# Optimization experiments

Hardware: AMD Instinct MI355X
Metric: run time of the kernel (lower is better)

## Reference

```python
import jax, jax.numpy as jnp
import numpy as np

H = 16  # n_head
EPS = 1e-12  # F.normalize eps


def l2norm(t):
    n = jnp.linalg.norm(t, axis=-1, keepdims=True)
    return t / jnp.maximum(n, EPS)


def setup_inputs() -> dict:
    key = jax.random.key(0)
    ks = jax.random.split(key, 12)
    B, T, C, K, N = 4, 1024, 1024, 16, 16384
    T_xl = 1024
    return {
        "x": jax.random.normal(ks[0], (B, T, C), jnp.float32),
        "xl_memory": jax.random.normal(ks[1], (B, T_xl, 2, C), jnp.float32),
        "relative_positions": jax.random.normal(ks[2], (H, T, T_xl + T), jnp.float32),
        "db": jax.random.normal(ks[3], (B, N, 2, C), jnp.float32),
        "knn_idx": jax.random.randint(ks[4], (B, T, K), 0, N, jnp.int32),
        "knn_mask": jnp.ones((B,), bool),
        "Wq": jax.random.normal(ks[5], (C, C), jnp.float32) * (C ** -0.5),
        "Wk": jax.random.normal(ks[6], (C, C), jnp.float32) * (C ** -0.5),
        "Wv": jax.random.normal(ks[7], (C, C), jnp.float32) * (C ** -0.5),
        "Wp": jax.random.normal(ks[8], (C, C), jnp.float32) * (C ** -0.5),
        "bp": jnp.zeros((C,), jnp.float32),
        "gate_bias": jax.random.normal(ks[9], (H, 1, 1), jnp.float32),
    }


def reference(x, xl_memory, relative_positions, db, knn_idx, knn_mask,
              Wq, Wk, Wv, Wp, bp, gate_bias):
    B, T, C = x.shape
    D = C // H
    scale = D ** -0.5

    # projections (torch Linear: y = x @ W.T), then L2-normalize q, k
    q = l2norm(jnp.einsum('btc,oc->bto', x, Wq))
    k = l2norm(jnp.einsum('btc,oc->bto', x, Wk))
    v = jnp.einsum('btc,oc->bto', x, Wv)

    k_xl, v_xl = xl_memory[..., 0, :], xl_memory[..., 1, :]
    k_full = jnp.concatenate((k_xl, k), axis=1)   # [B, j, C]
    v_full = jnp.concatenate((v_xl, v), axis=1)

    def to_heads(t):  # [B, S, C] -> [B, H, S, D]
        return t.reshape(B, t.shape[1], H, D).transpose(0, 2, 1, 3)

    qh, kh, vh = to_heads(q), to_heads(k_full), to_heads(v_full)
    i, j = T, k_full.shape[1]

    # XL attention with relative bias, scale applied AFTER bias (as in source)
    w = jnp.einsum('bhid,bhjd->bhij', qh, kh)
    w = (w + relative_positions[None, :, -i:, -j:]) * scale
    causal = jnp.triu(jnp.ones((i, j), bool), j - i + 1)
    w = jnp.where(causal, -jnp.inf, w)
    w = jax.nn.softmax(w, axis=-1)
    weighted_values = jnp.einsum('bhij,bhjd->bhid', w, vh)  # [B,H,T,D]

    # kNN memory attention: per-token gather of top-k (key,value) pairs
    mem_kv = db[jnp.arange(B)[:, None, None], knn_idx]      # [B,T,K,2,C]
    Kk = knn_idx.shape[-1]
    mem_k = mem_kv[..., 0, :].reshape(B, T, Kk, H, D).transpose(0, 3, 1, 2, 4)  # [B,H,T,K,D]
    mem_v = mem_kv[..., 1, :].reshape(B, T, Kk, H, D).transpose(0, 3, 1, 2, 4)
    mem_w = jnp.einsum('bhtd,bhtkd->bhtk', qh, mem_k) * scale
    mem_w = jax.nn.softmax(mem_w, axis=-1)
    mem_weighted = jnp.einsum('bhtk,bhtkd->bhtd', mem_w, mem_v)

    # per-head gated combination, then per-batch knn availability mask
    g = gate_bias[None]  # [1,H,1,1]
    combined = mem_weighted * g + weighted_values * (1.0 - g)
    combined = jnp.where(knn_mask[:, None, None, None], combined, weighted_values)

    out = combined.transpose(0, 2, 1, 3).reshape(B, T, C)
    out = jnp.einsum('btc,oc->bto', out, Wp) + bp

    # new XL memory: last T (normalized-k, v) pairs
    new_xl_memory = jnp.stack((k_full, v_full), axis=-2)[:, -T:]  # [B,T,2,C]
    return out, new_xl_memory
```

## Files before the change

kernel.cpp:

```cpp
#include <hip/hip_runtime.h>

typedef unsigned short u16;
typedef float f32x4 __attribute__((ext_vector_type(4)));
typedef u16 u16x4 __attribute__((ext_vector_type(4)));
typedef u16 u16x8 __attribute__((ext_vector_type(8)));
typedef __bf16 bf16x8 __attribute__((ext_vector_type(8)));

#define QSCALE 0.18033688011112043f

__device__ __forceinline__ u16 f2b(float f) {
    unsigned u = __float_as_uint(f);
    unsigned r = (u + 0x7fffu + ((u >> 16) & 1u)) >> 16;
    return (u16)r;
}

__device__ __forceinline__ float b2f(u16 v) {
    return __uint_as_float((unsigned)v << 16);
}

__device__ __forceinline__ int tile_ofs(int qb) {
    return 17 * qb + (qb * (qb - 1)) / 2;
}

__device__ __forceinline__ f32x4 mfma16(u16x8 a, u16x8 b, f32x4 c) {
    return __builtin_amdgcn_mfma_f32_16x16x32_bf16(
        __builtin_bit_cast(bf16x8, a), __builtin_bit_cast(bf16x8, b), c, 0, 0, 0);
}

__device__ __forceinline__ void gload_lds16(const void* g, void* l) {
    __builtin_amdgcn_global_load_lds(
        (const __attribute__((address_space(1))) void*)g,
        (__attribute__((address_space(3))) void*)l, 16, 0, 0);
}

__global__ __launch_bounds__(256) void convert_all_kernel(
    const float* __restrict__ x, const float* __restrict__ Wq,
    const float* __restrict__ Wk, const float* __restrict__ Wv,
    const float* __restrict__ Wp, const float* __restrict__ xl,
    const float* __restrict__ rel,
    u16* __restrict__ x_b, u16* __restrict__ Wcat, u16* __restrict__ Wpb,
    u16* __restrict__ kf, u16* __restrict__ vf, u16* __restrict__ relt) {
    int i = blockIdx.x * 256 + threadIdx.x;
    if (i < 4194304) {
        const float* src;
        u16* dst;
        if (i < 1048576) {
            src = x + 4 * (size_t)i;
            dst = x_b + 4 * (size_t)i;
        } else if (i < 1835008) {
            int j = i - 1048576;
            int sel = j >> 18, off = j & 262143;
            const float* s = sel == 0 ? Wq : sel == 1 ? Wk : Wv;
            src = s + 4 * (size_t)off;
            dst = Wcat + 4 * (size_t)j;
        } else if (i < 2097152) {
            int j = i - 1835008;
            src = Wp + 4 * (size_t)j;
            dst = Wpb + 4 * (size_t)j;
        } else {
            int j = i - 2097152;
            int c4 = j & 255, s = (j >> 8) & 1, t = (j >> 9) & 1023, b = j >> 19;
            src = xl + 4 * (size_t)j;
            dst = (s == 0 ? kf : vf) + ((size_t)b * 2048 + t) * 1024 + c4 * 4;
        }
        f32x4 v = *(const f32x4*)src;
        u16x4 o;
        o[0] = f2b(v[0]); o[1] = f2b(v[1]); o[2] = f2b(v[2]); o[3] = f2b(v[3]);
        *(u16x4*)dst = o;
    } else {
        int g = i - 4194304;
        int ftid = g & 255;
        int lin = g >> 8;
        int h = lin / 392;
        int lt = lin - h * 392;
        int qb = 0;
#pragma unroll
        for (int q = 1; q < 16; ++q)
            if (lt >= tile_ofs(q)) qb = q;
        int jt = lt - tile_ofs(qb);
        int w = ftid >> 6, lane = ftid & 63, g16 = lane >> 4, l16 = lane & 15;
        const float* rbase = rel + ((size_t)h * 1024 + qb * 64 + w * 16 + g16 * 4) * 2048
                                 + jt * 64 + l16;
        u16 vals[16];
#pragma unroll
        for (int nj = 0; nj < 4; ++nj)
#pragma unroll
            for (int r2 = 0; r2 < 4; ++r2)
                vals[nj * 4 + r2] = f2b(rbase[(size_t)r2 * 2048 + nj * 16] * QSCALE);
        u16* dstp = relt + ((size_t)lin * 256 + ftid) * 16;
        *(u16x8*)dstp = *(u16x8*)vals;
        *(u16x8*)(dstp + 8) = *(u16x8*)(vals + 8);
    }
}

__global__ __launch_bounds__(256) void gemm_bt_kernel(const u16* __restrict__ A,
                                                      const u16* __restrict__ B,
                                                      float* __restrict__ C,
                                                      u16* __restrict__ Cb,
                                                      int M, int N, int K,
                                                      const float* __restrict__ bias) {
    __shared__ u16 As[2][128 * 32];
    __shared__ u16 Bs[2][128 * 32];
    const int tid = threadIdx.x;
    const int w = tid >> 6, lane = tid & 63, g16 = lane >> 4, l16 = lane & 15;
    const int wr = w >> 1, wc = w & 1;
    const int m0 = blockIdx.y * 128, n0 = blockIdx.x * 128;

    f32x4 acc[4][4];
    f32x4 z4 = {0.f, 0.f, 0.f, 0.f};
#pragma unroll
    for (int mi = 0; mi < 4; ++mi)
#pragma unroll
        for (int nj = 0; nj < 4; ++nj) acc[mi][nj] = z4;

    const int r0 = tid >> 2;
    const int koff = (tid & 3) * 8;

    for (int k0 = 0; k0 < K; k0 += 64) {
#pragma unroll
        for (int half = 0; half < 2; ++half)
#pragma unroll
            for (int s = 0; s < 2; ++s) {
                int rr = r0 + 64 * s;
                gload_lds16(A + (size_t)(m0 + rr) * K + k0 + half * 32 + koff,
                            (char*)As[half] + w * 1024 + s * 4096);
                gload_lds16(B + (size_t)(n0 + rr) * K + k0 + half * 32 + koff,
                            (char*)Bs[half] + w * 1024 + s * 4096);
            }
        __syncthreads();
#pragma unroll
        for (int half = 0; half < 2; ++half) {
            u16x8 af[4], bfr[4];
#pragma unroll
            for (int x = 0; x < 4; ++x) {
                af[x]  = *(const u16x8*)&As[half][(wr * 64 + x * 16 + l16) * 32 + g16 * 8];
                bfr[x] = *(const u16x8*)&Bs[half][(wc * 64 + x * 16 + l16) * 32 + g16 * 8];
            }
#pragma unroll
            for (int mi = 0; mi < 4; ++mi)
#pragma unroll
                for (int nj = 0; nj < 4; ++nj)
                    acc[mi][nj] = mfma16(af[mi], bfr[nj], acc[mi][nj]);
        }
        __syncthreads();
    }

#pragma unroll
    for (int mi = 0; mi < 4; ++mi) {
        int row = m0 + wr * 64 + mi * 16 + g16 * 4;
#pragma unroll
        for (int nj = 0; nj < 4; ++nj) {
            int col = n0 + wc * 64 + nj * 16 + l16;
            if (Cb) {
#pragma unroll
                for (int rr = 0; rr < 4; ++rr)
                    Cb[(size_t)(row + rr) * N + col] = f2b(acc[mi][nj][rr]);
            } else {
                float bval = bias ? bias[col] : 0.0f;
#pragma unroll
                for (int rr = 0; rr < 4; ++rr)
                    C[(size_t)(row + rr) * N + col] = acc[mi][nj][rr] + bval;
            }
        }
    }
}

__global__ __launch_bounds__(256) void postproc_kernel(const u16* __restrict__ qkvb,
                                                       u16* __restrict__ qb16,
                                                       u16* __restrict__ kfull,
                                                       u16* __restrict__ vfull,
                                                       float* __restrict__ newxl) {
    int row = blockIdx.x;
    int b = row >> 10, t = row & 1023;
    int tid = threadIdx.x, w = tid >> 6, lane = tid & 63;
    const u16* qr = qkvb + (size_t)row * 3072;

    u16x4 q4 = ((const u16x4*)qr)[tid];
    u16x4 k4 = ((const u16x4*)(qr + 1024))[tid];
    u16x4 v4 = ((const u16x4*)(qr + 2048))[tid];
    float qa[4], ka[4], va[4];
    float sq = 0.f, sk = 0.f;
#pragma unroll
    for (int j = 0; j < 4; ++j) {
        qa[j] = b2f(q4[j]); sq += qa[j] * qa[j];
        ka[j] = b2f(k4[j]); sk += ka[j] * ka[j];
        va[j] = b2f(v4[j]);
    }
#pragma unroll
    for (int mk = 32; mk; mk >>= 1) {
        sq += __shfl_xor(sq, mk);
        sk += __shfl_xor(sk, mk);
    }
    __shared__ float red[2][4];
    if (lane == 0) { red[0][w] = sq; red[1][w] = sk; }
    __syncthreads();
    sq = red[0][0] + red[0][1] + red[0][2] + red[0][3];
    sk = red[1][0] + red[1][1] + red[1][2] + red[1][3];
    float rq = QSCALE / fmaxf(sqrtf(sq), 1e-12f);
    float rk = 1.0f / fmaxf(sqrtf(sk), 1e-12f);

    size_t orow = (size_t)row * 1024;
    size_t krow = ((size_t)b * 2048 + 1024 + t) * 1024;
    size_t xrow = (size_t)row * 2048;
    u16x4 qo, ko;
    f32x4 kx, vx;
#pragma unroll
    for (int j = 0; j < 4; ++j) {
        qo[j] = f2b(qa[j] * rq);
        float kv = ka[j] * rk;
        ko[j] = f2b(kv);
        kx[j] = kv;
        vx[j] = va[j];
    }
    ((u16x4*)(qb16 + orow))[tid] = qo;
    ((u16x4*)(kfull + krow))[tid] = ko;
    ((u16x4*)(vfull + krow))[tid] = v4;
    ((f32x4*)(newxl + xrow))[tid] = kx;
    ((f32x4*)(newxl + xrow + 1024))[tid] = vx;
}

__global__ __launch_bounds__(256) void flash_kernel(const u16* __restrict__ qb16,
                                                    const u16* __restrict__ kfull,
                                                    const u16* __restrict__ vfull,
                                                    const u16* __restrict__ relt,
                                                    u16* __restrict__ wvout) {
    const int qb = blockIdx.x, h = blockIdx.y, b = blockIdx.z;
    const int tid = threadIdx.x, w = tid >> 6, lane = tid & 63;
    const int g16 = lane >> 4, l16 = lane & 15;
    __shared__ u16 Ks[2][64 * 64];
    __shared__ u16 Vt[2][64 * 64];
    __shared__ u16 Ps[4][16 * 64];
    const int qi0 = qb * 64;

    {
        const u16* base = qb16 + ((size_t)(b * 1024 + qi0)) * 1024 + h * 64;
#pragma unroll
        for (int s = 0; s < 2; ++s) {
            int off = (tid + 256 * s) * 16;
            int r = off >> 7, cb = off & 127;
            int cbs = cb ^ ((r & 7) << 4);
            gload_lds16((const char*)(base + (size_t)r * 1024) + cbs,
                        (char*)Ks[0] + w * 1024 + s * 4096);
        }
    }
    __syncthreads();
    u16x8 qf[2];
#pragma unroll
    for (int ks = 0; ks < 2; ++ks) {
        int row = w * 16 + l16;
        int cb = (ks * 64 + g16 * 16) ^ ((row & 7) << 4);
        qf[ks] = *(const u16x8*)((const char*)Ks[0] + row * 128 + cb);
    }
    __syncthreads();

    auto stageK = [&](int buf, int j0) {
        const u16* kbase = kfull + ((size_t)b * 2048 + j0) * 1024 + h * 64;
#pragma unroll
        for (int s = 0; s < 2; ++s) {
            int off = (tid + 256 * s) * 16;
            int r = off >> 7, cb = off & 127;
            int cbs = cb ^ ((r & 7) << 4);
            gload_lds16((const char*)(kbase + (size_t)r * 1024) + cbs,
                        (char*)Ks[buf] + w * 1024 + s * 4096);
        }
    };
    const int jp = tid >> 3, d0v = (tid & 7) * 8;
    auto loadV = [&](int j0, u16x8* v0, u16x8* v1) {
        const u16* v0p = vfull + ((size_t)b * 2048 + j0 + 2 * jp) * 1024 + h * 64 + d0v;
        *v0 = *(const u16x8*)v0p;
        *v1 = *(const u16x8*)(v0p + 1024);
    };
    auto writeVt = [&](int buf, u16x8 v0, u16x8 v1) {
#pragma unroll
        for (int u = 0; u < 8; ++u) {
            int d = d0v + u;
            unsigned val = (unsigned)v0[u] | ((unsigned)v1[u] << 16);
            int bo = d * 128 + ((4 * jp) ^ ((d & 7) << 4));
            *(unsigned*)((char*)Vt[buf] + bo) = val;
        }
    };

    const u16* relp = relt + ((size_t)(h * 392 + tile_ofs(qb)) * 256 + tid) * 16;

    float l_r[4] = {0.f, 0.f, 0.f, 0.f};
    f32x4 accO[4];
    f32x4 z4 = {0.f, 0.f, 0.f, 0.f};
#pragma unroll
    for (int nd = 0; nd < 4; ++nd) accO[nd] = z4;

    const int ntiles = qb + 17;
    u16x8 v0n, v1n, rc0, rc1, rn0, rn1;

    stageK(0, 0);
    loadV(0, &v0n, &v1n);
    rc0 = *(const u16x8*)relp;
    rc1 = *(const u16x8*)(relp + 8);
    __syncthreads();
    writeVt(0, v0n, v1n);
    __syncthreads();

    int cur = 0;
    for (int jt = 0; jt < ntiles; ++jt) {
        const int j0 = jt * 64;
        const bool more = (jt + 1 < ntiles);
        if (more) {
            stageK(cur ^ 1, j0 + 64);
            loadV(j0 + 64, &v0n, &v1n);
            const u16* rp = relp + (size_t)(jt + 1) * 256 * 16;
            rn0 = *(const u16x8*)rp;
            rn1 = *(const u16x8*)(rp + 8);
        }

        f32x4 s4[4];
#pragma unroll
        for (int nj = 0; nj < 4; ++nj) {
            u16x8 rc = (nj < 2) ? rc0 : rc1;
            int base4 = (nj & 1) * 4;
            s4[nj][0] = b2f(rc[base4 + 0]);
            s4[nj][1] = b2f(rc[base4 + 1]);
            s4[nj][2] = b2f(rc[base4 + 2]);
            s4[nj][3] = b2f(rc[base4 + 3]);
#pragma unroll
            for (int ks = 0; ks < 2; ++ks) {
                int row = nj * 16 + l16;
                int cb = (ks * 64 + g16 * 16) ^ ((row & 7) << 4);
                u16x8 kf = *(const u16x8*)((const char*)Ks[cur] + row * 128 + cb);
                s4[nj] = mfma16(qf[ks], kf, s4[nj]);
            }
        }

        if (more) {
#pragma unroll
            for (int nj = 0; nj < 4; ++nj)
#pragma unroll
                for (int r2 = 0; r2 < 4; ++r2) {
                    float pe = exp2f(s4[nj][r2]);
                    l_r[r2] += pe;
                    int prow = g16 * 4 + r2;
                    int pbo = prow * 128 + (((nj * 16 + l16) * 2) ^ ((prow & 7) << 4));
                    *(u16*)((char*)Ps[w] + pbo) = __builtin_bit_cast(u16, (__bf16)pe);
                }
        } else {
#pragma unroll
            for (int nj = 0; nj < 4; ++nj) {
                int jg = j0 + nj * 16 + l16;
#pragma unroll
                for (int r2 = 0; r2 < 4; ++r2) {
                    int ig = qi0 + w * 16 + g16 * 4 + r2;
                    float pe = (jg > ig + 1024) ? 0.f : exp2f(s4[nj][r2]);
                    l_r[r2] += pe;
                    int prow = g16 * 4 + r2;
                    int pbo = prow * 128 + (((nj * 16 + l16) * 2) ^ ((prow & 7) << 4));
                    *(u16*)((char*)Ps[w] + pbo) = __builtin_bit_cast(u16, (__bf16)pe);
                }
            }
        }

#pragma unroll
        for (int ks = 0; ks < 2; ++ks) {
            int acb = (ks * 64 + g16 * 16) ^ ((l16 & 7) << 4);
            u16x8 pf = *(const u16x8*)((const char*)Ps[w] + l16 * 128 + acb);
#pragma unroll
            for (int nd = 0; nd < 4; ++nd) {
                int brow = nd * 16 + l16;
                int bcb = (ks * 64 + g16 * 16) ^ ((brow & 7) << 4);
                u16x8 vf = *(const u16x8*)((const char*)Vt[cur] + brow * 128 + bcb);
                accO[nd] = mfma16(pf, vf, accO[nd]);
            }
        }

        if (more) {
            writeVt(cur ^ 1, v0n, v1n);
            rc0 = rn0; rc1 = rn1;
        }
        __syncthreads();
        cur ^= 1;
    }

#pragma unroll
    for (int r2 = 0; r2 < 4; ++r2) {
#pragma unroll
        for (int mk = 1; mk < 16; mk <<= 1) l_r[r2] += __shfl_xor(l_r[r2], mk);
        l_r[r2] = __builtin_amdgcn_rcpf(l_r[r2]);
    }

#pragma unroll
    for (int nd = 0; nd < 4; ++nd)
#pragma unroll
        for (int r2 = 0; r2 < 4; ++r2) {
            int ig = qi0 + w * 16 + g16 * 4 + r2;
            int col = h * 64 + nd * 16 + l16;
            wvout[((size_t)b * 1024 + ig) * 1024 + col] = f2b(accO[nd][r2] * l_r[r2]);
        }
}

__global__ __launch_bounds__(256) void memgate_kernel(const u16* __restrict__ qb16,
                                                      const float* __restrict__ db,
                                                      const int* __restrict__ knn,
                                                      const u16* __restrict__ wvbuf,
                                                      const float* __restrict__ gate,
                                                      u16* __restrict__ comb) {
    int blk = blockIdx.x;
    int b = blk >> 10;
    int tid = threadIdx.x, w = tid >> 6, lane = tid & 63;
    int h = w * 4 + (lane >> 4);
    int l16 = lane & 15;
    int d0base = h * 64 + l16 * 4;
    size_t rowoff = (size_t)blk * 1024 + d0base;

    u16x4 qv = *(const u16x4*)(qb16 + rowoff);
    f32x4 q4;
    q4[0] = b2f(qv[0]); q4[1] = b2f(qv[1]); q4[2] = b2f(qv[2]); q4[3] = b2f(qv[3]);
    const int* kidx = knn + (size_t)blk * 16;

    float logit[16];
#pragma unroll
    for (int kk = 0; kk < 16; ++kk) {
        size_t roff = ((size_t)b * 16384 + kidx[kk]) * 2048 + d0base;
        f32x4 k4 = *(const f32x4*)(db + roff);
        float pp = q4[0] * k4[0] + q4[1] * k4[1] + q4[2] * k4[2] + q4[3] * k4[3];
        pp += __shfl_xor(pp, 1);
        pp += __shfl_xor(pp, 2);
        pp += __shfl_xor(pp, 4);
        pp += __shfl_xor(pp, 8);
        logit[kk] = pp;
    }
    float mx = -1e30f;
#pragma unroll
    for (int kk = 0; kk < 16; ++kk) mx = fmaxf(mx, logit[kk]);
    float ssum = 0.f;
    float pr[16];
#pragma unroll
    for (int kk = 0; kk < 16; ++kk) {
        pr[kk] = exp2f(logit[kk] - mx);
        ssum += pr[kk];
    }
    float inv = __builtin_amdgcn_rcpf(ssum);
    f32x4 acc = {0.f, 0.f, 0.f, 0.f};
#pragma unroll
    for (int kk = 0; kk < 16; ++kk) {
        size_t roff = ((size_t)b * 16384 + kidx[kk]) * 2048 + 1024 + d0base;
        f32x4 v4 = *(const f32x4*)(db + roff);
        float pw = pr[kk] * inv;
        acc[0] += pw * v4[0];
        acc[1] += pw * v4[1];
        acc[2] += pw * v4[2];
        acc[3] += pw * v4[3];
    }
    u16x4 wv4 = *(const u16x4*)(wvbuf + rowoff);
    float g = gate[h];
    u16x4 o;
#pragma unroll
    for (int j = 0; j < 4; ++j) o[j] = f2b(acc[j] * g + b2f(wv4[j]) * (1.f - g));
    *(u16x4*)(comb + rowoff) = o;
}

extern "C" void kernel_launch(void* const* d_in, const int* in_sizes, int n_in,
                              void* d_out, int out_size, void* d_ws, size_t ws_size,
                              hipStream_t stream) {
    const float* x    = (const float*)d_in[0];
    const float* xl   = (const float*)d_in[1];
    const float* rel  = (const float*)d_in[2];
    const float* db   = (const float*)d_in[3];
    const int*   knn  = (const int*)d_in[4];
    const float* Wq   = (const float*)d_in[6];
    const float* Wk   = (const float*)d_in[7];
    const float* Wv   = (const float*)d_in[8];
    const float* Wp   = (const float*)d_in[9];
    const float* bp   = (const float*)d_in[10];
    const float* gate = (const float*)d_in[11];

    float* out   = (float*)d_out;
    float* newxl = out + (size_t)4 * 1024 * 1024;

    char* p = (char*)d_ws;
    auto alloc = [&](size_t bytes) {
        char* q = p;
        p += (bytes + 255) & ~(size_t)255;
        return q;
    };
    u16*   x_b    = (u16*)alloc((size_t)4096 * 1024 * 2);
    u16*   Wcat_b = (u16*)alloc((size_t)3072 * 1024 * 2);
    u16*   Wp_b   = (u16*)alloc((size_t)1024 * 1024 * 2);
    u16*   rel_t  = (u16*)alloc((size_t)16 * 392 * 256 * 16 * 2);
    u16*   qkvb   = (u16*)alloc((size_t)4096 * 3072 * 2);
    u16*   q_b    = (u16*)alloc((size_t)4096 * 1024 * 2);
    u16*   kf_b   = (u16*)alloc((size_t)4 * 2048 * 1024 * 2);
    u16*   vf_b   = (u16*)alloc((size_t)4 * 2048 * 1024 * 2);
    u16*   wvb    = (u16*)alloc((size_t)4096 * 1024 * 2);
    u16*   comb   = (u16*)alloc((size_t)4096 * 1024 * 2);

    convert_all_kernel<<<22656, 256, 0, stream>>>(x, Wq, Wk, Wv, Wp, xl, rel,
                                                  x_b, Wcat_b, Wp_b, kf_b, vf_b, rel_t);

    gemm_bt_kernel<<<dim3(24, 32), 256, 0, stream>>>(x_b, Wcat_b, nullptr, qkvb,
                                                     4096, 3072, 1024, nullptr);
    postproc_kernel<<<4096, 256, 0, stream>>>(qkvb, q_b, kf_b, vf_b, newxl);
    flash_kernel<<<dim3(16, 16, 4), 256, 0, stream>>>(q_b, kf_b, vf_b, rel_t, wvb);
    memgate_kernel<<<4096, 256, 0, stream>>>(q_b, db, knn, wvb, gate, comb);
    gemm_bt_kernel<<<dim3(8, 32), 256, 0, stream>>>(comb, Wp_b, out, nullptr,
                                                    4096, 1024, 1024, bp);
}
```

Before: 334.1 us.

## Co-schedule flash and kNN memory attention in one launch, fuse gating into output GEMM

Merges the flash attention kernel and the kNN memory gather kernel into a single launch. One block in five runs flash attention and the rest run memory attention, so the compute-heavy and gather-bound work can overlap on the GPU. The memory path now writes only the gate-scaled memory output. The gate blend with the XL attention output is moved into the A-tile load of the output projection GEMM, which removes the separate combined buffer. The cost is that the GEMM A tile is now built with register loads and conversions instead of direct-to-LDS loads, and the two block types have mismatched resource needs inside one kernel.

```diff
diff --git a/kernel.cpp b/kernel.cpp
--- a/kernel.cpp
+++ b/kernel.cpp
@@ -95,10 +95,8 @@
 
 __global__ __launch_bounds__(256) void gemm_bt_kernel(const u16* __restrict__ A,
                                                       const u16* __restrict__ B,
-                                                      float* __restrict__ C,
                                                       u16* __restrict__ Cb,
-                                                      int M, int N, int K,
-                                                      const float* __restrict__ bias) {
+                                                      int M, int N, int K) {
     __shared__ u16 As[2][128 * 32];
     __shared__ u16 Bs[2][128 * 32];
     const int tid = threadIdx.x;
@@ -151,16 +149,83 @@
 #pragma unroll
         for (int nj = 0; nj < 4; ++nj) {
             int col = n0 + wc * 64 + nj * 16 + l16;
-            if (Cb) {
-#pragma unroll
-                for (int rr = 0; rr < 4; ++rr)
-                    Cb[(size_t)(row + rr) * N + col] = f2b(acc[mi][nj][rr]);
-            } else {
-                float bval = bias ? bias[col] : 0.0f;
-#pragma unroll
-                for (int rr = 0; rr < 4; ++rr)
-                    C[(size_t)(row + rr) * N + col] = acc[mi][nj][rr] + bval;
-            }
+#pragma unroll
+            for (int rr = 0; rr < 4; ++rr)
+                Cb[(size_t)(row + rr) * N + col] = f2b(acc[mi][nj][rr]);
+        }
+    }
+}
+
+__global__ __launch_bounds__(256) void gemm_out_kernel(const u16* __restrict__ Amem,
+                                                       const u16* __restrict__ Awv,
+                                                       const float* __restrict__ gate,
+                                                       const u16* __restrict__ B,
+                                                       float* __restrict__ C,
+                                                       int M, int N, int K,
+                                                       const float* __restrict__ bias) {
+    __shared__ u16 As[2][128 * 32];
+    __shared__ u16 Bs[2][128 * 32];
+    const int tid = threadIdx.x;
+    const int w = tid >> 6, lane = tid & 63, g16 = lane >> 4, l16 = lane & 15;
+    const int wr = w >> 1, wc = w & 1;
+    const int m0 = blockIdx.y * 128, n0 = blockIdx.x * 128;
+
+    f32x4 acc[4][4];
+    f32x4 z4 = {0.f, 0.f, 0.f, 0.f};
+#pragma unroll
+    for (int mi = 0; mi < 4; ++mi)
+#pragma unroll
+        for (int nj = 0; nj < 4; ++nj) acc[mi][nj] = z4;
+
+    const int r0 = tid >> 2;
+    const int koff = (tid & 3) * 8;
+
+    for (int k0 = 0; k0 < K; k0 += 64) {
+        float om = 1.0f - gate[k0 >> 6];
+#pragma unroll
+        for (int half = 0; half < 2; ++half)
+#pragma unroll
+            for (int s = 0; s < 2; ++s) {
+                int rr = r0 + 64 * s;
+                size_t ao = (size_t)(m0 + rr) * K + k0 + half * 32 + koff;
+                u16x8 am = *(const u16x8*)(Amem + ao);
+                u16x8 aw = *(const u16x8*)(Awv + ao);
+                u16x8 ac;
+#pragma unroll
+                for (int j = 0; j < 8; ++j)
+                    ac[j] = f2b(b2f(am[j]) + om * b2f(aw[j]));
+                *(u16x8*)((char*)As[half] + w * 1024 + s * 4096 + (lane) * 16) = ac;
+                gload_lds16(B + (size_t)(n0 + rr) * K + k0 + half * 32 + koff,
+                            (char*)Bs[half] + w * 1024 + s * 4096);
+            }
+        __syncthreads();
+#pragma unroll
+        for (int half = 0; half < 2; ++half) {
+            u16x8 af[4], bfr[4];
+#pragma unroll
+            for (int x = 0; x < 4; ++x) {
+                af[x]  = *(const u16x8*)&As[half][(wr * 64 + x * 16 + l16) * 32 + g16 * 8];
+                bfr[x] = *(const u16x8*)&Bs[half][(wc * 64 + x * 16 + l16) * 32 + g16 * 8];
+            }
+#pragma unroll
+            for (int mi = 0; mi < 4; ++mi)
+#pragma unroll
+                for (int nj = 0; nj < 4; ++nj)
+                    acc[mi][nj] = mfma16(af[mi], bfr[nj], acc[mi][nj]);
+        }
+        __syncthreads();
+    }
+
+#pragma unroll
+    for (int mi = 0; mi < 4; ++mi) {
+        int row = m0 + wr * 64 + mi * 16 + g16 * 4;
+#pragma unroll
+        for (int nj = 0; nj < 4; ++nj) {
+            int col = n0 + wc * 64 + nj * 16 + l16;
+            float bval = bias[col];
+#pragma unroll
+            for (int rr = 0; rr < 4; ++rr)
+                C[(size_t)(row + rr) * N + col] = acc[mi][nj][rr] + bval;
         }
     }
 }
@@ -178,13 +243,12 @@
     u16x4 q4 = ((const u16x4*)qr)[tid];
     u16x4 k4 = ((const u16x4*)(qr + 1024))[tid];
     u16x4 v4 = ((const u16x4*)(qr + 2048))[tid];
-    float qa[4], ka[4], va[4];
+    float qa[4], ka[4];
     float sq = 0.f, sk = 0.f;
 #pragma unroll
     for (int j = 0; j < 4; ++j) {
         qa[j] = b2f(q4[j]); sq += qa[j] * qa[j];
         ka[j] = b2f(k4[j]); sk += ka[j] * ka[j];
-        va[j] = b2f(v4[j]);
     }
 #pragma unroll
     for (int mk = 32; mk; mk >>= 1) {
@@ -210,7 +274,7 @@
         float kv = ka[j] * rk;
         ko[j] = f2b(kv);
         kx[j] = kv;
-        vx[j] = va[j];
+        vx[j] = b2f(v4[j]);
     }
     ((u16x4*)(qb16 + orow))[tid] = qo;
     ((u16x4*)(kfull + krow))[tid] = ko;
@@ -219,240 +283,240 @@
     ((f32x4*)(newxl + xrow + 1024))[tid] = vx;
 }
 
-__global__ __launch_bounds__(256) void flash_kernel(const u16* __restrict__ qb16,
-                                                    const u16* __restrict__ kfull,
-                                                    const u16* __restrict__ vfull,
-                                                    const u16* __restrict__ relt,
-                                                    u16* __restrict__ wvout) {
-    const int qb = blockIdx.x, h = blockIdx.y, b = blockIdx.z;
-    const int tid = threadIdx.x, w = tid >> 6, lane = tid & 63;
-    const int g16 = lane >> 4, l16 = lane & 15;
+__global__ __launch_bounds__(256) void fused_attn_kernel(const u16* __restrict__ qb16,
+                                                         const u16* __restrict__ kfull,
+                                                         const u16* __restrict__ vfull,
+                                                         const u16* __restrict__ relt,
+                                                         u16* __restrict__ wvout,
+                                                         const float* __restrict__ db,
+                                                         const int* __restrict__ knn,
+                                                         const float* __restrict__ gate,
+                                                         u16* __restrict__ membg) {
     __shared__ u16 Ks[2][64 * 64];
     __shared__ u16 Vt[2][64 * 64];
     __shared__ u16 Ps[4][16 * 64];
-    const int qi0 = qb * 64;
-
-    {
-        const u16* base = qb16 + ((size_t)(b * 1024 + qi0)) * 1024 + h * 64;
-#pragma unroll
-        for (int s = 0; s < 2; ++s) {
-            int off = (tid + 256 * s) * 16;
-            int r = off >> 7, cb = off & 127;
-            int cbs = cb ^ ((r & 7) << 4);
-            gload_lds16((const char*)(base + (size_t)r * 1024) + cbs,
-                        (char*)Ks[0] + w * 1024 + s * 4096);
-        }
-    }
-    __syncthreads();
-    u16x8 qf[2];
-#pragma unroll
-    for (int ks = 0; ks < 2; ++ks) {
-        int row = w * 16 + l16;
-        int cb = (ks * 64 + g16 * 16) ^ ((row & 7) << 4);
-        qf[ks] = *(const u16x8*)((const char*)Ks[0] + row * 128 + cb);
-    }
-    __syncthreads();
-
-    auto stageK = [&](int buf, int j0) {
-        const u16* kbase = kfull + ((size_t)b * 2048 + j0) * 1024 + h * 64;
-#pragma unroll
-        for (int s = 0; s < 2; ++s) {
-            int off = (tid + 256 * s) * 16;
-            int r = off >> 7, cb = off & 127;
-            int cbs = cb ^ ((r & 7) << 4);
-            gload_lds16((const char*)(kbase + (size_t)r * 1024) + cbs,
-                        (char*)Ks[buf] + w * 1024 + s * 4096);
-        }
-    };
-    const int jp = tid >> 3, d0v = (tid & 7) * 8;
-    auto loadV = [&](int j0, u16x8* v0, u16x8* v1) {
-        const u16* v0p = vfull + ((size_t)b * 2048 + j0 + 2 * jp) * 1024 + h * 64 + d0v;
-        *v0 = *(const u16x8*)v0p;
-        *v1 = *(const u16x8*)(v0p + 1024);
-    };
-    auto writeVt = [&](int buf, u16x8 v0, u16x8 v1) {
-#pragma unroll
-        for (int u = 0; u < 8; ++u) {
-            int d = d0v + u;
-            unsigned val = (unsigned)v0[u] | ((unsigned)v1[u] << 16);
-            int bo = d * 128 + ((4 * jp) ^ ((d & 7) << 4));
-            *(unsigned*)((char*)Vt[buf] + bo) = val;
-        }
-    };
-
-    const u16* relp = relt + ((size_t)(h * 392 + tile_ofs(qb)) * 256 + tid) * 16;
-
-    float l_r[4] = {0.f, 0.f, 0.f, 0.f};
-    f32x4 accO[4];
-    f32x4 z4 = {0.f, 0.f, 0.f, 0.f};
-#pragma unroll
-    for (int nd = 0; nd < 4; ++nd) accO[nd] = z4;
-
-    const int ntiles = qb + 17;
-    u16x8 v0n, v1n, rc0, rc1, rn0, rn1;
-
-    stageK(0, 0);
-    loadV(0, &v0n, &v1n);
-    rc0 = *(const u16x8*)relp;
-    rc1 = *(const u16x8*)(relp + 8);
-    __syncthreads();
-    writeVt(0, v0n, v1n);
-    __syncthreads();
-
-    int cur = 0;
-    for (int jt = 0; jt < ntiles; ++jt) {
-        const int j0 = jt * 64;
-        const bool more = (jt + 1 < ntiles);
-        if (more) {
-            stageK(cur ^ 1, j0 + 64);
-            loadV(j0 + 64, &v0n, &v1n);
-            const u16* rp = relp + (size_t)(jt + 1) * 256 * 16;
-            rn0 = *(const u16x8*)rp;
-            rn1 = *(const u16x8*)(rp + 8);
-        }
-
-        f32x4 s4[4];
-#pragma unroll
-        for (int nj = 0; nj < 4; ++nj) {
-            u16x8 rc = (nj < 2) ? rc0 : rc1;
-            int base4 = (nj & 1) * 4;
-            s4[nj][0] = b2f(rc[base4 + 0]);
-            s4[nj][1] = b2f(rc[base4 + 1]);
-            s4[nj][2] = b2f(rc[base4 + 2]);
-            s4[nj][3] = b2f(rc[base4 + 3]);
+    const int bi = blockIdx.x;
+    const int tid = threadIdx.x, w = tid >> 6, lane = tid & 63;
+
+    if (bi % 5 == 0) {
+        const int f = bi / 5;
+        const int qb = f & 15, h = (f >> 4) & 15, b = f >> 8;
+        const int g16 = lane >> 4, l16 = lane & 15;
+        const int qi0 = qb * 64;
+
+        {
+            const u16* base = qb16 + ((size_t)(b * 1024 + qi0)) * 1024 + h * 64;
+#pragma unroll
+            for (int s = 0; s < 2; ++s) {
+                int off = (tid + 256 * s) * 16;
+                int r = off >> 7, cb = off & 127;
+                int cbs = cb ^ ((r & 7) << 4);
+                gload_lds16((const char*)(base + (size_t)r * 1024) + cbs,
+                            (char*)Ks[0] + w * 1024 + s * 4096);
+            }
+        }
+        __syncthreads();
+        u16x8 qf[2];
+#pragma unroll
+        for (int ks = 0; ks < 2; ++ks) {
+            int row = w * 16 + l16;
+            int cb = (ks * 64 + g16 * 16) ^ ((row & 7) << 4);
+            qf[ks] = *(const u16x8*)((const char*)Ks[0] + row * 128 + cb);
+        }
+        __syncthreads();
+
+        auto stageK = [&](int buf, int j0) {
+            const u16* kbase = kfull + ((size_t)b * 2048 + j0) * 1024 + h * 64;
+#pragma unroll
+            for (int s = 0; s < 2; ++s) {
+                int off = (tid + 256 * s) * 16;
+                int r = off >> 7, cb = off & 127;
+                int cbs = cb ^ ((r & 7) << 4);
+                gload_lds16((const char*)(kbase + (size_t)r * 1024) + cbs,
+                            (char*)Ks[buf] + w * 1024 + s * 4096);
+            }
+        };
+        const int jp = tid >> 3, d0v = (tid & 7) * 8;
+        auto loadV = [&](int j0, u16x8* v0, u16x8* v1) {
+            const u16* v0p = vfull + ((size_t)b * 2048 + j0 + 2 * jp) * 1024 + h * 64 + d0v;
+            *v0 = *(const u16x8*)v0p;
+            *v1 = *(const u16x8*)(v0p + 1024);
+        };
+        auto writeVt = [&](int buf, u16x8 v0, u16x8 v1) {
+#pragma unroll
+            for (int u = 0; u < 8; ++u) {
+                int d = d0v + u;
+                unsigned val = (unsigned)v0[u] | ((unsigned)v1[u] << 16);
+                int bo = d * 128 + ((4 * jp) ^ ((d & 7) << 4));
+                *(unsigned*)((char*)Vt[buf] + bo) = val;
+            }
+        };
+
+        const u16* relp = relt + ((size_t)(h * 392 + tile_ofs(qb)) * 256 + tid) * 16;
+
+        float l_r[4] = {0.f, 0.f, 0.f, 0.f};
+        f32x4 accO[4];
+        f32x4 z4 = {0.f, 0.f, 0.f, 0.f};
+#pragma unroll
+        for (int nd = 0; nd < 4; ++nd) accO[nd] = z4;
+
+        const int ntiles = qb + 17;
+        u16x8 v0n, v1n, rc0, rc1, rn0, rn1;
+
+        stageK(0, 0);
+        loadV(0, &v0n, &v1n);
+        rc0 = *(const u16x8*)relp;
+        rc1 = *(const u16x8*)(relp + 8);
+        __syncthreads();
+        writeVt(0, v0n, v1n);
+        __syncthreads();
+
+        int cur = 0;
+        for (int jt = 0; jt < ntiles; ++jt) {
+            const int j0 = jt * 64;
+            const bool more = (jt + 1 < ntiles);
+            if (more) {
+                stageK(cur ^ 1, j0 + 64);
+                loadV(j0 + 64, &v0n, &v1n);
+                const u16* rp = relp + (size_t)(jt + 1) * 256 * 16;
+                rn0 = *(const u16x8*)rp;
+                rn1 = *(const u16x8*)(rp + 8);
+            }
+
+            f32x4 s4[4];
+#pragma unroll
+            for (int nj = 0; nj < 4; ++nj) {
+                u16x8 rc = (nj < 2) ? rc0 : rc1;
+                int base4 = (nj & 1) * 4;
+                s4[nj][0] = b2f(rc[base4 + 0]);
+                s4[nj][1] = b2f(rc[base4 + 1]);
+                s4[nj][2] = b2f(rc[base4 + 2]);
+                s4[nj][3] = b2f(rc[base4 + 3]);
+#pragma unroll
+                for (int ks = 0; ks < 2; ++ks) {
+                    int row = nj * 16 + l16;
+                    int cb = (ks * 64 + g16 * 16) ^ ((row & 7) << 4);
+                    u16x8 kf = *(const u16x8*)((const char*)Ks[cur] + row * 128 + cb);
+                    s4[nj] = mfma16(qf[ks], kf, s4[nj]);
+                }
+            }
+
+            if (more) {
+#pragma unroll
+                for (int nj = 0; nj < 4; ++nj)
+#pragma unroll
+                    for (int r2 = 0; r2 < 4; ++r2) {
+                        float pe = exp2f(s4[nj][r2]);
+                        l_r[r2] += pe;
+                        int prow = g16 * 4 + r2;
+                        int pbo = prow * 128 + (((nj * 16 + l16) * 2) ^ ((prow & 7) << 4));
+                        *(u16*)((char*)Ps[w] + pbo) = __builtin_bit_cast(u16, (__bf16)pe);
+                    }
+            } else {
+#pragma unroll
+                for (int nj = 0; nj < 4; ++nj) {
+                    int jg = j0 + nj * 16 + l16;
+#pragma unroll
+                    for (int r2 = 0; r2 < 4; ++r2) {
+                        int ig = qi0 + w * 16 + g16 * 4 + r2;
+                        float pe = (jg > ig + 1024) ? 0.f : exp2f(s4[nj][r2]);
+                        l_r[r2] += pe;
+                        int prow = g16 * 4 + r2;
+                        int pbo = prow * 128 + (((nj * 16 + l16) * 2) ^ ((prow & 7) << 4));
+                        *(u16*)((char*)Ps[w] + pbo) = __builtin_bit_cast(u16, (__bf16)pe);
+                    }
+                }
+            }
+
 #pragma unroll
             for (int ks = 0; ks < 2; ++ks) {
-                int row = nj * 16 + l16;
-                int cb = (ks * 64 + g16 * 16) ^ ((row & 7) << 4);
-                u16x8 kf = *(const u16x8*)((const char*)Ks[cur] + row * 128 + cb);
-                s4[nj] = mfma16(qf[ks], kf, s4[nj]);
-            }
-        }
-
-        if (more) {
-#pragma unroll
-            for (int nj = 0; nj < 4; ++nj)
-#pragma unroll
-                for (int r2 = 0; r2 < 4; ++r2) {
-                    float pe = exp2f(s4[nj][r2]);
-                    l_r[r2] += pe;
-                    int prow = g16 * 4 + r2;
-                    int pbo = prow * 128 + (((nj * 16 + l16) * 2) ^ ((prow & 7) << 4));
-                    *(u16*)((char*)Ps[w] + pbo) = __builtin_bit_cast(u16, (__bf16)pe);
+                int acb = (ks * 64 + g16 * 16) ^ ((l16 & 7) << 4);
+                u16x8 pf = *(const u16x8*)((const char*)Ps[w] + l16 * 128 + acb);
+#pragma unroll
+                for (int nd = 0; nd < 4; ++nd) {
+                    int brow = nd * 16 + l16;
+                    int bcb = (ks * 64 + g16 * 16) ^ ((brow & 7) << 4);
+                    u16x8 vf = *(const u16x8*)((const char*)Vt[cur] + brow * 128 + bcb);
+                    accO[nd] = mfma16(pf, vf, accO[nd]);
                 }
-        } else {
-#pragma unroll
-            for (int nj = 0; nj < 4; ++nj) {
-                int jg = j0 + nj * 16 + l16;
-#pragma unroll
-                for (int r2 = 0; r2 < 4; ++r2) {
-                    int ig = qi0 + w * 16 + g16 * 4 + r2;
-                    float pe = (jg > ig + 1024) ? 0.f : exp2f(s4[nj][r2]);
-                    l_r[r2] += pe;
-                    int prow = g16 * 4 + r2;
-                    int pbo = prow * 128 + (((nj * 16 + l16) * 2) ^ ((prow & 7) << 4));
-                    *(u16*)((char*)Ps[w] + pbo) = __builtin_bit_cast(u16, (__bf16)pe);
-                }
-            }
-        }
-
-#pragma unroll
-        for (int ks = 0; ks < 2; ++ks) {
-            int acb = (ks * 64 + g16 * 16) ^ ((l16 & 7) << 4);
-            u16x8 pf = *(const u16x8*)((const char*)Ps[w] + l16 * 128 + acb);
-#pragma unroll
-            for (int nd = 0; nd < 4; ++nd) {
-                int brow = nd * 16 + l16;
-                int bcb = (ks * 64 + g16 * 16) ^ ((brow & 7) << 4);
-                u16x8 vf = *(const u16x8*)((const char*)Vt[cur] + brow * 128 + bcb);
-                accO[nd] = mfma16(pf, vf, accO[nd]);
-            }
-        }
-
-        if (more) {
-            writeVt(cur ^ 1, v0n, v1n);
-            rc0 = rn0; rc1 = rn1;
-        }
-        __syncthreads();
-        cur ^= 1;
-    }
-
-#pragma unroll
-    for (int r2 = 0; r2 < 4; ++r2) {
-#pragma unroll
-        for (int mk = 1; mk < 16; mk <<= 1) l_r[r2] += __shfl_xor(l_r[r2], mk);
-        l_r[r2] = __builtin_amdgcn_rcpf(l_r[r2]);
-    }
-
-#pragma unroll
-    for (int nd = 0; nd < 4; ++nd)
+            }
+
+            if (more) {
+                writeVt(cur ^ 1, v0n, v1n);
+                rc0 = rn0; rc1 = rn1;
+            }
+            __syncthreads();
+            cur ^= 1;
+        }
+
 #pragma unroll
         for (int r2 = 0; r2 < 4; ++r2) {
-            int ig = qi0 + w * 16 + g16 * 4 + r2;
-            int col = h * 64 + nd * 16 + l16;
-            wvout[((size_t)b * 1024 + ig) * 1024 + col] = f2b(accO[nd][r2] * l_r[r2]);
-        }
-}
-
-__global__ __launch_bounds__(256) void memgate_kernel(const u16* __restrict__ qb16,
-                                                      const float* __restrict__ db,
-                                                      const int* __restrict__ knn,
-                                                      const u16* __restrict__ wvbuf,
-                                                      const float* __restrict__ gate,
-                                                      u16* __restrict__ comb) {
-    int blk = blockIdx.x;
-    int b = blk >> 10;
-    int tid = threadIdx.x, w = tid >> 6, lane = tid & 63;
-    int h = w * 4 + (lane >> 4);
-    int l16 = lane & 15;
-    int d0base = h * 64 + l16 * 4;
-    size_t rowoff = (size_t)blk * 1024 + d0base;
-
-    u16x4 qv = *(const u16x4*)(qb16 + rowoff);
-    f32x4 q4;
-    q4[0] = b2f(qv[0]); q4[1] = b2f(qv[1]); q4[2] = b2f(qv[2]); q4[3] = b2f(qv[3]);
-    const int* kidx = knn + (size_t)blk * 16;
-
-    float logit[16];
-#pragma unroll
-    for (int kk = 0; kk < 16; ++kk) {
-        size_t roff = ((size_t)b * 16384 + kidx[kk]) * 2048 + d0base;
-        f32x4 k4 = *(const f32x4*)(db + roff);
-        float pp = q4[0] * k4[0] + q4[1] * k4[1] + q4[2] * k4[2] + q4[3] * k4[3];
-        pp += __shfl_xor(pp, 1);
-        pp += __shfl_xor(pp, 2);
-        pp += __shfl_xor(pp, 4);
-        pp += __shfl_xor(pp, 8);
-        logit[kk] = pp;
-    }
-    float mx = -1e30f;
-#pragma unroll
-    for (int kk = 0; kk < 16; ++kk) mx = fmaxf(mx, logit[kk]);
-    float ssum = 0.f;
-    float pr[16];
-#pragma unroll
-    for (int kk = 0; kk < 16; ++kk) {
-        pr[kk] = exp2f(logit[kk] - mx);
-        ssum += pr[kk];
-    }
-    float inv = __builtin_amdgcn_rcpf(ssum);
-    f32x4 acc = {0.f, 0.f, 0.f, 0.f};
-#pragma unroll
-    for (int kk = 0; kk < 16; ++kk) {
-        size_t roff = ((size_t)b * 16384 + kidx[kk]) * 2048 + 1024 + d0base;
-        f32x4 v4 = *(const f32x4*)(db + roff);
-        float pw = pr[kk] * inv;
-        acc[0] += pw * v4[0];
-        acc[1] += pw * v4[1];
-        acc[2] += pw * v4[2];
-        acc[3] += pw * v4[3];
-    }
-    u16x4 wv4 = *(const u16x4*)(wvbuf + rowoff);
-    float g = gate[h];
-    u16x4 o;
-#pragma unroll
-    for (int j = 0; j < 4; ++j) o[j] = f2b(acc[j] * g + b2f(wv4[j]) * (1.f - g));
-    *(u16x4*)(comb + rowoff) = o;
+#pragma unroll
+            for (int mk = 1; mk < 16; mk <<= 1) l_r[r2] += __shfl_xor(l_r[r2], mk);
+            l_r[r2] = __builtin_amdgcn_rcpf(l_r[r2]);
+        }
+
+#pragma unroll
+        for (int nd = 0; nd < 4; ++nd)
+#pragma unroll
+            for (int r2 = 0; r2 < 4; ++r2) {
+                int ig = qi0 + w * 16 + g16 * 4 + r2;
+                int col = h * 64 + nd * 16 + l16;
+                wvout[((size_t)b * 1024 + ig) * 1024 + col] = f2b(accO[nd][r2] * l_r[r2]);
+            }
+    } else {
+        int blk = bi - bi / 5 - 1;
+        int b = blk >> 10;
+        int h = w * 4 + (lane >> 4);
+        int l16 = lane & 15;
+        int d0base = h * 64 + l16 * 4;
+        size_t rowoff = (size_t)blk * 1024 + d0base;
+
+        u16x4 qv = *(const u16x4*)(qb16 + rowoff);
+        f32x4 q4;
+        q4[0] = b2f(qv[0]); q4[1] = b2f(qv[1]); q4[2] = b2f(qv[2]); q4[3] = b2f(qv[3]);
+        const int* kidx = knn + (size_t)blk * 16;
+
+        float logit[16];
+#pragma unroll
+        for (int kk = 0; kk < 16; ++kk) {
+            size_t roff = ((size_t)b * 16384 + kidx[kk]) * 2048 + d0base;
+            f32x4 k4 = *(const f32x4*)(db + roff);
+            float pp = q4[0] * k4[0] + q4[1] * k4[1] + q4[2] * k4[2] + q4[3] * k4[3];
+            pp += __shfl_xor(pp, 1);
+            pp += __shfl_xor(pp, 2);
+            pp += __shfl_xor(pp, 4);
+            pp += __shfl_xor(pp, 8);
+            logit[kk] = pp;
+        }
+        float mx = -1e30f;
+#pragma unroll
+        for (int kk = 0; kk < 16; ++kk) mx = fmaxf(mx, logit[kk]);
+        float ssum = 0.f;
+        float pr[16];
+#pragma unroll
+        for (int kk = 0; kk < 16; ++kk) {
+            pr[kk] = exp2f(logit[kk] - mx);
+            ssum += pr[kk];
+        }
+        float inv = __builtin_amdgcn_rcpf(ssum);
+        f32x4 acc = {0.f, 0.f, 0.f, 0.f};
+#pragma unroll
+        for (int kk = 0; kk < 16; ++kk) {
+            size_t roff = ((size_t)b * 16384 + kidx[kk]) * 2048 + 1024 + d0base;
+            f32x4 v4 = *(const f32x4*)(db + roff);
+            float pw = pr[kk] * inv;
+            acc[0] += pw * v4[0];
+            acc[1] += pw * v4[1];
+            acc[2] += pw * v4[2];
+            acc[3] += pw * v4[3];
+        }
+        float g = gate[h];
+        u16x4 o;
+#pragma unroll
+        for (int j = 0; j < 4; ++j) o[j] = f2b(acc[j] * g);
+        *(u16x4*)(membg + rowoff) = o;
+    }
 }
 
 extern "C" void kernel_launch(void* const* d_in, const int* in_sizes, int n_in,
@@ -488,16 +552,15 @@
     u16*   kf_b   = (u16*)alloc((size_t)4 * 2048 * 1024 * 2);
     u16*   vf_b   = (u16*)alloc((size_t)4 * 2048 * 1024 * 2);
     u16*   wvb    = (u16*)alloc((size_t)4096 * 1024 * 2);
-    u16*   comb   = (u16*)alloc((size_t)4096 * 1024 * 2);
+    u16*   membg  = (u16*)alloc((size_t)4096 * 1024 * 2);
 
     convert_all_kernel<<<22656, 256, 0, stream>>>(x, Wq, Wk, Wv, Wp, xl, rel,
                                                   x_b, Wcat_b, Wp_b, kf_b, vf_b, rel_t);
 
-    gemm_bt_kernel<<<dim3(24, 32), 256, 0, stream>>>(x_b, Wcat_b, nullptr, qkvb,
-                                                     4096, 3072, 1024, nullptr);
+    gemm_bt_kernel<<<dim3(24, 32), 256, 0, stream>>>(x_b, Wcat_b, qkvb, 4096, 3072, 1024);
     postproc_kernel<<<4096, 256, 0, stream>>>(qkvb, q_b, kf_b, vf_b, newxl);
-    flash_kernel<<<dim3(16, 16, 4), 256, 0, stream>>>(q_b, kf_b, vf_b, rel_t, wvb);
-    memgate_kernel<<<4096, 256, 0, stream>>>(q_b, db, knn, wvb, gate, comb);
-    gemm_bt_kernel<<<dim3(8, 32), 256, 0, stream>>>(comb, Wp_b, out, nullptr,
-                                                    4096, 1024, 1024, bp);
-}
+    fused_attn_kernel<<<5120, 256, 0, stream>>>(q_b, kf_b, vf_b, rel_t, wvb,
+                                                db, knn, gate, membg);
+    gemm_out_kernel<<<dim3(8, 32), 256, 0, stream>>>(membg, wvb, gate, Wp_b, out,
+                                                     4096, 1024, 1024, bp);
+}
```

New measurement: 325.7 us. 2.5% less time.
